# Kernel tuning notes

Measured on AMD Instinct MI355X. Metric: run time of the kernel, lower is better.

## Reference

```python
import jax, jax.numpy as jnp
import numpy as np

B, N, D, H, C, K = 4096, 64, 128, 256, 8, 3
L = N * D  # latent_dim = num_patches * d_model = 8192
UQ, LQ = 0.9, 0.1


def setup_inputs() -> dict:
    key = jax.random.key(0)
    ks = jax.random.split(key, 6)
    z = jax.random.normal(ks[0], (B, N, D), dtype=jnp.float32)
    q = jax.random.uniform(ks[1], (B,), dtype=jnp.float32)
    ch_ids = jax.random.randint(ks[2], (B,), 0, C, dtype=jnp.int32)
    # Xavier-style init for the 3 expert MLPs (Linear(L,H), Linear(H,L)) + heads Linear(L,1)
    s1 = float(np.sqrt(2.0 / (L + H)))
    s2 = float(np.sqrt(2.0 / (H + L)))
    sh = float(np.sqrt(2.0 / (L + 1)))
    W1 = jax.random.normal(ks[3], (K, L, H), dtype=jnp.float32) * s1
    W2 = jax.random.normal(ks[4], (K, H, L), dtype=jnp.float32) * s2
    Wh = jax.random.normal(ks[5], (K, L), dtype=jnp.float32) * sh
    return dict(z=z, q=q, ch_ids=ch_ids,
                W1=W1, b1=jnp.zeros((K, H), jnp.float32),
                W2=W2, b2=jnp.zeros((K, L), jnp.float32),
                Wh=Wh, bh=jnp.zeros((K,), jnp.float32))


def _channel_thresholds(q, ch_ids):
    """Per-channel sample-adjusted upper/lower quantiles, torch.quantile(..., interpolation='lower')."""
    def one(c):
        mask = ch_ids == c
        n = jnp.sum(mask).astype(jnp.float32)
        s = jnp.sort(jnp.where(mask, q, jnp.inf))  # channel values occupy first n slots
        au = jnp.ceil((n + 1.0) * UQ) / n
        pu = jnp.where(au > 1.0, UQ, au)
        al = jnp.floor((n + 1.0) * LQ) / n
        pl = jnp.where(al < 0.0, LQ, al)
        iu = jnp.floor(pu * (n - 1.0)).astype(jnp.int32)  # 'lower' interpolation index
        il = jnp.floor(pl * (n - 1.0)).astype(jnp.int32)
        return s[iu], s[il]
    return jax.vmap(one)(jnp.arange(C))  # (C,), (C,)


def reference(z, q, ch_ids, W1, b1, W2, b2, Wh, bh):
    uq_th, lq_th = _channel_thresholds(q, ch_ids)
    group = jnp.where(q <= lq_th[ch_ids], 2,
                      jnp.where(q >= uq_th[ch_ids], 0, 1)).astype(jnp.int32)  # (B,)
    zf = z.reshape(z.shape[0], -1)  # (B, L) -- Flatten(start_dim=-2)

    def expert(w1, c1, w2, c2, wh, ch):
        h = jax.nn.gelu(zf @ w1 + c1, approximate=False)   # (B, H)
        o = h @ w2 + c2                                     # (B, L)
        return o @ wh + ch                                  # (B,)

    logits_all = jax.vmap(expert)(W1, b1, W2, b2, Wh, bh)   # (K, B)
    logits = jnp.take_along_axis(logits_all, group[None, :], axis=0)[0]  # (B,)

    # per-channel softmax over logits (stable), matching torch.softmax on each channel's indices
    m = jax.ops.segment_max(logits, ch_ids, num_segments=C)
    e = jnp.exp(logits - m[ch_ids])
    ssum = jax.ops.segment_sum(e, ch_ids, num_segments=C)
    qwa_coeff = e / ssum[ch_ids]
    refined_probs = q * qwa_coeff
    return refined_probs
```

## Files before the change

### kernel.cpp

```cpp
#include <hip/hip_runtime.h>

typedef unsigned short u16;
typedef unsigned int u32;
typedef __attribute__((ext_vector_type(8))) short short8;
typedef __attribute__((ext_vector_type(4))) float f32x4;

#define NB 4096
#define LDIM 8192
#define HDIM 256
#define NEXP 3
#define NCH 8
#define KSPLIT 4
#define KSLICE (LDIM / KSPLIT)
#define BK 64
#define NT (KSLICE / BK)

__device__ inline u16 f2bf(float f) {
  u32 u = __float_as_uint(f);
  u += 0x7FFFu + ((u >> 16) & 1u);
  return (u16)(u >> 16);
}
__device__ inline u32 pack2(float x, float y) {
  return (u32)f2bf(x) | ((u32)f2bf(y) << 16);
}
__device__ inline void gll16(const void* g, void* l) {
  __builtin_amdgcn_global_load_lds((const __attribute__((address_space(1))) void*)g,
                                   (__attribute__((address_space(3))) void*)l, 16, 0, 0);
}

__global__ void thresh_kernel(const float* __restrict__ q, const int* __restrict__ ch,
                              float* __restrict__ uq_th, float* __restrict__ lq_th) {
  int c = blockIdx.x;
  int tid = threadIdx.x;
  __shared__ float vals[1536];
  __shared__ int oidx[1536];
  __shared__ int n_sh;
  if (tid == 0) n_sh = 0;
  __syncthreads();
  for (int i = tid; i < NB; i += 256) {
    if (ch[i] == c) {
      int p = atomicAdd(&n_sh, 1);
      if (p < 1536) { vals[p] = q[i]; oidx[p] = i; }
    }
  }
  __syncthreads();
  int n = n_sh < 1536 ? n_sh : 1536;
  float nf = (float)n_sh;
  float au = ceilf((nf + 1.0f) * 0.9f) / nf;
  float pu = (au > 1.0f) ? 0.9f : au;
  int iu = (int)floorf(pu * (nf - 1.0f));
  float al = floorf((nf + 1.0f) * 0.1f) / nf;
  float pl = (al < 0.0f) ? 0.1f : al;
  int il = (int)floorf(pl * (nf - 1.0f));
  for (int e = tid; e < n; e += 256) {
    float v = vals[e];
    int oi = oidx[e];
    int r = 0;
    for (int m = 0; m < n; ++m) {
      float vm = vals[m];
      if (vm < v || (vm == v && oidx[m] < oi)) r++;
    }
    if (r == iu) uq_th[c] = v;
    if (r == il) lq_th[c] = v;
  }
}

__global__ void group_kernel(const float* __restrict__ q, const int* __restrict__ ch,
                             const float* __restrict__ uq_th, const float* __restrict__ lq_th,
                             int* __restrict__ group, int* __restrict__ cnt, int* __restrict__ idxl) {
  int b = blockIdx.x * 256 + threadIdx.x;
  if (b >= NB) return;
  float qq = q[b];
  int c = ch[b];
  int g = (qq <= lq_th[c]) ? 2 : ((qq >= uq_th[c]) ? 0 : 1);
  group[b] = g;
  int pos = atomicAdd(&cnt[g], 1);
  idxl[g * NB + pos] = b;
}

__global__ void v_kernel(const float* __restrict__ W2, const float* __restrict__ Wh,
                         float* __restrict__ v) {
  int wv = blockIdx.x * 4 + (threadIdx.x >> 6);
  int lane = threadIdx.x & 63;
  int k = wv >> 8, h = wv & 255;
  const float4* w2 = (const float4*)(W2 + ((size_t)k * HDIM + h) * LDIM);
  const float4* wh = (const float4*)(Wh + (size_t)k * LDIM);
  float s = 0.f;
  for (int i = lane; i < LDIM / 4; i += 64) {
    float4 a = w2[i], b = wh[i];
    s += a.x * b.x + a.y * b.y + a.z * b.z + a.w * b.w;
  }
  for (int off = 32; off; off >>= 1) s += __shfl_down(s, off);
  if (lane == 0) v[k * HDIM + h] = s;
}

__global__ void cbias_kernel(const float* __restrict__ b2, const float* __restrict__ Wh,
                             const float* __restrict__ bh, float* __restrict__ cbias) {
  int k = threadIdx.x >> 6, lane = threadIdx.x & 63;
  float s = 0.f;
  for (int l = lane; l < LDIM; l += 64) s += b2[k * LDIM + l] * Wh[k * LDIM + l];
  for (int off = 32; off; off >>= 1) s += __shfl_down(s, off);
  if (lane == 0) cbias[k] = s + bh[k];
}

__global__ void transpose_kernel(const float* __restrict__ W1, u16* __restrict__ W1t) {
  __shared__ float tile[64][65];
  int k = blockIdx.z;
  int l0 = blockIdx.x * 64;
  int h0 = blockIdx.y * 64;
  int t = threadIdx.x;
  const float* src = W1 + (size_t)k * LDIM * HDIM + (size_t)l0 * HDIM + h0;
  u16* dst = W1t + (size_t)k * HDIM * LDIM + (size_t)h0 * LDIM + l0;
  int hr = t & 63, lr = t >> 6;
#pragma unroll
  for (int p = 0; p < 16; ++p) {
    int l = p * 4 + lr;
    tile[l][hr] = src[(size_t)l * HDIM + hr];
  }
  __syncthreads();
  int cw = t & 7, hw = t >> 3;
#pragma unroll
  for (int p = 0; p < 2; ++p) {
    int h = p * 32 + hw;
    short8 v8;
#pragma unroll
    for (int j = 0; j < 8; ++j) v8[j] = (short)f2bf(tile[cw * 8 + j][h]);
    *(short8*)&dst[(size_t)h * LDIM + cw * 8] = v8;
  }
}

__global__ void __launch_bounds__(256) gemm_kernel(
    const float* __restrict__ z, const u16* __restrict__ W1t,
    const int* __restrict__ idxl, const int* __restrict__ cnt,
    float* __restrict__ part) {
  int zid = blockIdx.z;
  int kexp = zid >> 2, s = zid & 3;
  int nk = cnt[kexp];
  int rowbase = blockIdx.x * 64;
  if (rowbase >= nk) return;
  int h0 = blockIdx.y * 64;
  int tid = threadIdx.x;
  int lane = tid & 63, wv = tid >> 6;

  __shared__ __align__(16) u16 As[2][4096];
  __shared__ __align__(16) u16 Bs[2][4096];
  __shared__ int sidx[64];

  const int* idxk = idxl + kexp * NB;
  if (tid < 64) {
    int p = rowbase + tid;
    sidx[tid] = idxk[p < nk ? p : nk - 1];
  }

  int r0 = tid >> 3, r1 = r0 + 32, kg = tid & 7;
  int p0 = rowbase + r0; if (p0 > nk - 1) p0 = nk - 1;
  int p1 = rowbase + r1; if (p1 > nk - 1) p1 = nk - 1;
  size_t kbase = (size_t)s * KSLICE;
  const float* zr0 = z + (size_t)idxk[p0] * LDIM + kbase + kg * 8;
  const float* zr1 = z + (size_t)idxk[p1] * LDIM + kbase + kg * 8;
  int swA0 = r0 * 64 + ((kg * 8) ^ ((r0 & 7) * 8));
  int swA1 = r1 * 64 + ((kg * 8) ^ ((r1 & 7) * 8));

  const u16* bsrc0 = W1t + ((size_t)kexp * HDIM + h0 + wv * 16 + (lane >> 3)) * LDIM +
                     kbase + (size_t)(((lane & 7) ^ (lane >> 3)) * 8);
  const u16* bsrc1 = bsrc0 + 8 * LDIM;

  int fr = lane & 15, kgl = (lane >> 4) * 8;
  int wr = (wv >> 1) * 32, wc = (wv & 1) * 32;
  int ra0 = wr + fr, ra1 = ra0 + 16, ca0 = wc + fr, ca1 = ca0 + 16;
  int xA0 = (ra0 & 7) * 8, xA1 = (ra1 & 7) * 8, xB0 = (ca0 & 7) * 8, xB1 = (ca1 & 7) * 8;

  f32x4 acc[2][2] = {};
  float4 a0, a1, a2, a3;

  {
    char* lb = (char*)&Bs[0][0] + wv * 2048;
    gll16(bsrc0, lb);
    gll16(bsrc1, lb + 1024);
    a0 = *(const float4*)(zr0);
    a1 = *(const float4*)(zr0 + 4);
    a2 = *(const float4*)(zr1);
    a3 = *(const float4*)(zr1 + 4);
    uint4 pa0, pa1;
    pa0.x = pack2(a0.x, a0.y); pa0.y = pack2(a0.z, a0.w);
    pa0.z = pack2(a1.x, a1.y); pa0.w = pack2(a1.z, a1.w);
    pa1.x = pack2(a2.x, a2.y); pa1.y = pack2(a2.z, a2.w);
    pa1.z = pack2(a3.x, a3.y); pa1.w = pack2(a3.z, a3.w);
    *(uint4*)&As[0][swA0] = pa0;
    *(uint4*)&As[0][swA1] = pa1;
  }
  __syncthreads();

  int cur = 0;
  for (int t = 0; t < NT; ++t) {
    int nxt = cur ^ 1;
    bool pre = (t + 1 < NT);
    if (pre) {
      int off = (t + 1) * BK;
      char* lb = (char*)&Bs[nxt][0] + wv * 2048;
      gll16(bsrc0 + off, lb);
      gll16(bsrc1 + off, lb + 1024);
      a0 = *(const float4*)(zr0 + off);
      a1 = *(const float4*)(zr0 + off + 4);
      a2 = *(const float4*)(zr1 + off);
      a3 = *(const float4*)(zr1 + off + 4);
    }
    const u16* Ac = &As[cur][0];
    const u16* Bc = &Bs[cur][0];
#pragma unroll
    for (int ks = 0; ks < 2; ++ks) {
      int kk = ks * 32 + kgl;
      short8 af0 = *(const short8*)&Ac[ra0 * 64 + (kk ^ xA0)];
      short8 af1 = *(const short8*)&Ac[ra1 * 64 + (kk ^ xA1)];
      short8 bf0 = *(const short8*)&Bc[ca0 * 64 + (kk ^ xB0)];
      short8 bf1 = *(const short8*)&Bc[ca1 * 64 + (kk ^ xB1)];
      acc[0][0] = __builtin_amdgcn_mfma_f32_16x16x32_bf16(af0, bf0, acc[0][0], 0, 0, 0);
      acc[0][1] = __builtin_amdgcn_mfma_f32_16x16x32_bf16(af0, bf1, acc[0][1], 0, 0, 0);
      acc[1][0] = __builtin_amdgcn_mfma_f32_16x16x32_bf16(af1, bf0, acc[1][0], 0, 0, 0);
      acc[1][1] = __builtin_amdgcn_mfma_f32_16x16x32_bf16(af1, bf1, acc[1][1], 0, 0, 0);
    }
    if (pre) {
      uint4 pa0, pa1;
      pa0.x = pack2(a0.x, a0.y); pa0.y = pack2(a0.z, a0.w);
      pa0.z = pack2(a1.x, a1.y); pa0.w = pack2(a1.z, a1.w);
      pa1.x = pack2(a2.x, a2.y); pa1.y = pack2(a2.z, a2.w);
      pa1.z = pack2(a3.x, a3.y); pa1.w = pack2(a3.z, a3.w);
      *(uint4*)&As[nxt][swA0] = pa0;
      *(uint4*)&As[nxt][swA1] = pa1;
    }
    __syncthreads();
    cur = nxt;
  }

  float* pdst = part + (size_t)s * NB * HDIM;
#pragma unroll
  for (int rb = 0; rb < 2; ++rb)
#pragma unroll
    for (int cb = 0; cb < 2; ++cb)
#pragma unroll
      for (int i = 0; i < 4; ++i) {
        int row = wr + rb * 16 + (lane >> 4) * 4 + i;
        int col = wc + cb * 16 + fr;
        if (rowbase + row < nk)
          pdst[(size_t)sidx[row] * HDIM + h0 + col] = acc[rb][cb][i];
      }
}

__global__ void ep_kernel(const float* __restrict__ part, const float* __restrict__ b1,
                          const float* __restrict__ v, const int* __restrict__ group,
                          float* __restrict__ logits) {
  int b = blockIdx.x;
  int t = threadIdx.x;
  int g = group[b];
  size_t o = (size_t)b * HDIM + t;
  const size_t SS = (size_t)NB * HDIM;
  float x = part[o] + part[o + SS] + part[o + 2 * SS] + part[o + 3 * SS] + b1[g * HDIM + t];
  float ge = 0.5f * x * (1.0f + erff(x * 0.70710678118654752f));
  float y = ge * v[g * HDIM + t];
#pragma unroll
  for (int off = 32; off; off >>= 1) y += __shfl_down(y, off);
  __shared__ float red[4];
  int lane = t & 63, wv = t >> 6;
  if (lane == 0) red[wv] = y;
  __syncthreads();
  if (t == 0) logits[b] = red[0] + red[1] + red[2] + red[3];
}

__global__ void softmax_kernel(const float* __restrict__ logits, const float* __restrict__ cbias,
                               const int* __restrict__ group, const float* __restrict__ q,
                               const int* __restrict__ ch, float* __restrict__ out) {
  int c = blockIdx.x;
  int tid = threadIdx.x;
  __shared__ float red[256];
  float m = -3.4e38f;
  for (int i = tid; i < NB; i += 256)
    if (ch[i] == c) {
      float x = logits[i] + cbias[group[i]];
      m = fmaxf(m, x);
    }
  red[tid] = m;
  __syncthreads();
  for (int s = 128; s > 0; s >>= 1) {
    if (tid < s) red[tid] = fmaxf(red[tid], red[tid + s]);
    __syncthreads();
  }
  m = red[0];
  __syncthreads();
  float sum = 0.f;
  for (int i = tid; i < NB; i += 256)
    if (ch[i] == c) sum += expf(logits[i] + cbias[group[i]] - m);
  red[tid] = sum;
  __syncthreads();
  for (int s = 128; s > 0; s >>= 1) {
    if (tid < s) red[tid] += red[tid + s];
    __syncthreads();
  }
  float S = red[0];
  for (int i = tid; i < NB; i += 256)
    if (ch[i] == c) out[i] = q[i] * expf(logits[i] + cbias[group[i]] - m) / S;
}

extern "C" void kernel_launch(void* const* d_in, const int* in_sizes, int n_in,
                              void* d_out, int out_size, void* d_ws, size_t ws_size,
                              hipStream_t stream) {
  const float* z  = (const float*)d_in[0];
  const float* q  = (const float*)d_in[1];
  const int*   ch = (const int*)d_in[2];
  const float* W1 = (const float*)d_in[3];
  const float* b1 = (const float*)d_in[4];
  const float* W2 = (const float*)d_in[5];
  const float* b2 = (const float*)d_in[6];
  const float* Wh = (const float*)d_in[7];
  const float* bh = (const float*)d_in[8];
  float* out = (float*)d_out;

  float* wsf    = (float*)d_ws;
  float* logits = wsf;
  int*   cnt    = (int*)(wsf + 4096);
  float* uq_th  = wsf + 4100;
  float* lq_th  = wsf + 4108;
  float* cbias  = wsf + 4116;
  float* v      = wsf + 4120;
  int*   group  = (int*)(wsf + 4888);
  int*   idxl   = (int*)(wsf + 8984);
  u16*   W1t    = (u16*)(wsf + 21272);
  float* part   = wsf + 3167000;

  hipMemsetAsync((char*)d_ws + 4096 * 4, 0, 16, stream);
  hipLaunchKernelGGL(thresh_kernel, dim3(NCH), dim3(256), 0, stream, q, ch, uq_th, lq_th);
  hipLaunchKernelGGL(group_kernel, dim3(16), dim3(256), 0, stream, q, ch, uq_th, lq_th, group, cnt, idxl);
  hipLaunchKernelGGL(v_kernel, dim3(192), dim3(256), 0, stream, W2, Wh, v);
  hipLaunchKernelGGL(cbias_kernel, dim3(1), dim3(192), 0, stream, b2, Wh, bh, cbias);
  hipLaunchKernelGGL(transpose_kernel, dim3(128, 4, 3), dim3(256), 0, stream, W1, W1t);
  hipLaunchKernelGGL(gemm_kernel, dim3(64, 4, NEXP * KSPLIT), dim3(256), 0, stream,
                     z, W1t, idxl, cnt, part);
  hipLaunchKernelGGL(ep_kernel, dim3(NB), dim3(256), 0, stream, part, b1, v, group, logits);
  hipLaunchKernelGGL(softmax_kernel, dim3(NCH), dim3(256), 0, stream, logits, cbias, group, q, ch, out);
}
```

Baseline: 542.2 us.

## Halve GEMM K-tile and raise split-K to eight slices when workspace allows

The gather-GEMM's K tile shrinks from 64 to 32, which halves LDS per block and gives each thread one A row chunk and one B load instead of two. A new swizzle matches the narrower tile. The split-K factor becomes a runtime value, eight when the workspace is large enough, to put more blocks in flight. The cost is more partial-sum traffic in the epilogue, which now loops over the slices, plus one sync per 32-wide step, so the fixed overhead per MFMA rises.

```diff
diff --git a/kernel.cpp b/kernel.cpp
--- a/kernel.cpp
+++ b/kernel.cpp
@@ -10,10 +10,7 @@
 #define HDIM 256
 #define NEXP 3
 #define NCH 8
-#define KSPLIT 4
-#define KSLICE (LDIM / KSPLIT)
-#define BK 64
-#define NT (KSLICE / BK)
+#define BK 32
 
 __device__ inline u16 f2bf(float f) {
   u32 u = __float_as_uint(f);
@@ -132,9 +129,9 @@
 __global__ void __launch_bounds__(256) gemm_kernel(
     const float* __restrict__ z, const u16* __restrict__ W1t,
     const int* __restrict__ idxl, const int* __restrict__ cnt,
-    float* __restrict__ part) {
+    float* __restrict__ part, int nsl, int nt) {
   int zid = blockIdx.z;
-  int kexp = zid >> 2, s = zid & 3;
+  int kexp = zid / nsl, s = zid - kexp * nsl;
   int nk = cnt[kexp];
   int rowbase = blockIdx.x * 64;
   if (rowbase >= nk) return;
@@ -142,8 +139,8 @@
   int tid = threadIdx.x;
   int lane = tid & 63, wv = tid >> 6;
 
-  __shared__ __align__(16) u16 As[2][4096];
-  __shared__ __align__(16) u16 Bs[2][4096];
+  __shared__ __align__(16) u16 As[2][2048];
+  __shared__ __align__(16) u16 Bs[2][2048];
   __shared__ int sidx[64];
 
   const int* idxk = idxl + kexp * NB;
@@ -152,81 +149,66 @@
     sidx[tid] = idxk[p < nk ? p : nk - 1];
   }
 
-  int r0 = tid >> 3, r1 = r0 + 32, kg = tid & 7;
-  int p0 = rowbase + r0; if (p0 > nk - 1) p0 = nk - 1;
-  int p1 = rowbase + r1; if (p1 > nk - 1) p1 = nk - 1;
-  size_t kbase = (size_t)s * KSLICE;
-  const float* zr0 = z + (size_t)idxk[p0] * LDIM + kbase + kg * 8;
-  const float* zr1 = z + (size_t)idxk[p1] * LDIM + kbase + kg * 8;
-  int swA0 = r0 * 64 + ((kg * 8) ^ ((r0 & 7) * 8));
-  int swA1 = r1 * 64 + ((kg * 8) ^ ((r1 & 7) * 8));
-
-  const u16* bsrc0 = W1t + ((size_t)kexp * HDIM + h0 + wv * 16 + (lane >> 3)) * LDIM +
-                     kbase + (size_t)(((lane & 7) ^ (lane >> 3)) * 8);
-  const u16* bsrc1 = bsrc0 + 8 * LDIM;
+  int row = tid >> 2, kg = tid & 3;
+  int p0 = rowbase + row; if (p0 > nk - 1) p0 = nk - 1;
+  int kslice = nt * BK;
+  size_t kbase = (size_t)s * kslice;
+  const float* zr = z + (size_t)idxk[p0] * LDIM + kbase + kg * 8;
+  int sch = kg ^ ((row >> 1) & 3);
+  int swA = row * BK + sch * 8;
+
+  const u16* bsrc = W1t + ((size_t)kexp * HDIM + h0 + row) * LDIM + kbase + sch * 8;
 
   int fr = lane & 15, kgl = (lane >> 4) * 8;
+  int kc = kgl >> 3;
   int wr = (wv >> 1) * 32, wc = (wv & 1) * 32;
   int ra0 = wr + fr, ra1 = ra0 + 16, ca0 = wc + fr, ca1 = ca0 + 16;
-  int xA0 = (ra0 & 7) * 8, xA1 = (ra1 & 7) * 8, xB0 = (ca0 & 7) * 8, xB1 = (ca1 & 7) * 8;
+  int oA0 = ra0 * BK + (kc ^ ((ra0 >> 1) & 3)) * 8;
+  int oA1 = ra1 * BK + (kc ^ ((ra1 >> 1) & 3)) * 8;
+  int oB0 = ca0 * BK + (kc ^ ((ca0 >> 1) & 3)) * 8;
+  int oB1 = ca1 * BK + (kc ^ ((ca1 >> 1) & 3)) * 8;
 
   f32x4 acc[2][2] = {};
-  float4 a0, a1, a2, a3;
-
+  float4 a0, a1;
+
+  gll16(bsrc, (char*)&Bs[0][0] + wv * 1024);
+  a0 = *(const float4*)(zr);
+  a1 = *(const float4*)(zr + 4);
   {
-    char* lb = (char*)&Bs[0][0] + wv * 2048;
-    gll16(bsrc0, lb);
-    gll16(bsrc1, lb + 1024);
-    a0 = *(const float4*)(zr0);
-    a1 = *(const float4*)(zr0 + 4);
-    a2 = *(const float4*)(zr1);
-    a3 = *(const float4*)(zr1 + 4);
-    uint4 pa0, pa1;
-    pa0.x = pack2(a0.x, a0.y); pa0.y = pack2(a0.z, a0.w);
-    pa0.z = pack2(a1.x, a1.y); pa0.w = pack2(a1.z, a1.w);
-    pa1.x = pack2(a2.x, a2.y); pa1.y = pack2(a2.z, a2.w);
-    pa1.z = pack2(a3.x, a3.y); pa1.w = pack2(a3.z, a3.w);
-    *(uint4*)&As[0][swA0] = pa0;
-    *(uint4*)&As[0][swA1] = pa1;
+    uint4 pa;
+    pa.x = pack2(a0.x, a0.y); pa.y = pack2(a0.z, a0.w);
+    pa.z = pack2(a1.x, a1.y); pa.w = pack2(a1.z, a1.w);
+    *(uint4*)&As[0][swA] = pa;
   }
   __syncthreads();
 
   int cur = 0;
-  for (int t = 0; t < NT; ++t) {
+  for (int t = 0; t < nt; ++t) {
     int nxt = cur ^ 1;
-    bool pre = (t + 1 < NT);
+    bool pre = (t + 1 < nt);
     if (pre) {
       int off = (t + 1) * BK;
-      char* lb = (char*)&Bs[nxt][0] + wv * 2048;
-      gll16(bsrc0 + off, lb);
-      gll16(bsrc1 + off, lb + 1024);
-      a0 = *(const float4*)(zr0 + off);
-      a1 = *(const float4*)(zr0 + off + 4);
-      a2 = *(const float4*)(zr1 + off);
-      a3 = *(const float4*)(zr1 + off + 4);
-    }
-    const u16* Ac = &As[cur][0];
-    const u16* Bc = &Bs[cur][0];
-#pragma unroll
-    for (int ks = 0; ks < 2; ++ks) {
-      int kk = ks * 32 + kgl;
-      short8 af0 = *(const short8*)&Ac[ra0 * 64 + (kk ^ xA0)];
-      short8 af1 = *(const short8*)&Ac[ra1 * 64 + (kk ^ xA1)];
-      short8 bf0 = *(const short8*)&Bc[ca0 * 64 + (kk ^ xB0)];
-      short8 bf1 = *(const short8*)&Bc[ca1 * 64 + (kk ^ xB1)];
+      gll16(bsrc + off, (char*)&Bs[nxt][0] + wv * 1024);
+      a0 = *(const float4*)(zr + off);
+      a1 = *(const float4*)(zr + off + 4);
+    }
+    {
+      const u16* Ac = &As[cur][0];
+      const u16* Bc = &Bs[cur][0];
+      short8 af0 = *(const short8*)&Ac[oA0];
+      short8 af1 = *(const short8*)&Ac[oA1];
+      short8 bf0 = *(const short8*)&Bc[oB0];
+      short8 bf1 = *(const short8*)&Bc[oB1];
       acc[0][0] = __builtin_amdgcn_mfma_f32_16x16x32_bf16(af0, bf0, acc[0][0], 0, 0, 0);
       acc[0][1] = __builtin_amdgcn_mfma_f32_16x16x32_bf16(af0, bf1, acc[0][1], 0, 0, 0);
       acc[1][0] = __builtin_amdgcn_mfma_f32_16x16x32_bf16(af1, bf0, acc[1][0], 0, 0, 0);
       acc[1][1] = __builtin_amdgcn_mfma_f32_16x16x32_bf16(af1, bf1, acc[1][1], 0, 0, 0);
     }
     if (pre) {
-      uint4 pa0, pa1;
-      pa0.x = pack2(a0.x, a0.y); pa0.y = pack2(a0.z, a0.w);
-      pa0.z = pack2(a1.x, a1.y); pa0.w = pack2(a1.z, a1.w);
-      pa1.x = pack2(a2.x, a2.y); pa1.y = pack2(a2.z, a2.w);
-      pa1.z = pack2(a3.x, a3.y); pa1.w = pack2(a3.z, a3.w);
-      *(uint4*)&As[nxt][swA0] = pa0;
-      *(uint4*)&As[nxt][swA1] = pa1;
+      uint4 pa;
+      pa.x = pack2(a0.x, a0.y); pa.y = pack2(a0.z, a0.w);
+      pa.z = pack2(a1.x, a1.y); pa.w = pack2(a1.z, a1.w);
+      *(uint4*)&As[nxt][swA] = pa;
     }
     __syncthreads();
     cur = nxt;
@@ -239,22 +221,23 @@
     for (int cb = 0; cb < 2; ++cb)
 #pragma unroll
       for (int i = 0; i < 4; ++i) {
-        int row = wr + rb * 16 + (lane >> 4) * 4 + i;
+        int r = wr + rb * 16 + (lane >> 4) * 4 + i;
         int col = wc + cb * 16 + fr;
-        if (rowbase + row < nk)
-          pdst[(size_t)sidx[row] * HDIM + h0 + col] = acc[rb][cb][i];
+        if (rowbase + r < nk)
+          pdst[(size_t)sidx[r] * HDIM + h0 + col] = acc[rb][cb][i];
       }
 }
 
 __global__ void ep_kernel(const float* __restrict__ part, const float* __restrict__ b1,
                           const float* __restrict__ v, const int* __restrict__ group,
-                          float* __restrict__ logits) {
+                          float* __restrict__ logits, int nsl) {
   int b = blockIdx.x;
   int t = threadIdx.x;
   int g = group[b];
   size_t o = (size_t)b * HDIM + t;
   const size_t SS = (size_t)NB * HDIM;
-  float x = part[o] + part[o + SS] + part[o + 2 * SS] + part[o + 3 * SS] + b1[g * HDIM + t];
+  float x = b1[g * HDIM + t];
+  for (int i = 0; i < nsl; ++i) x += part[o + i * SS];
   float ge = 0.5f * x * (1.0f + erff(x * 0.70710678118654752f));
   float y = ge * v[g * HDIM + t];
 #pragma unroll
@@ -326,14 +309,18 @@
   u16*   W1t    = (u16*)(wsf + 21272);
   float* part   = wsf + 3167000;
 
+  size_t need8 = (size_t)3167000 * 4 + (size_t)8 * NB * HDIM * 4;
+  int nsl = (ws_size >= need8) ? 8 : 4;
+  int nt = (LDIM / nsl) / BK;
+
   hipMemsetAsync((char*)d_ws + 4096 * 4, 0, 16, stream);
   hipLaunchKernelGGL(thresh_kernel, dim3(NCH), dim3(256), 0, stream, q, ch, uq_th, lq_th);
   hipLaunchKernelGGL(group_kernel, dim3(16), dim3(256), 0, stream, q, ch, uq_th, lq_th, group, cnt, idxl);
   hipLaunchKernelGGL(v_kernel, dim3(192), dim3(256), 0, stream, W2, Wh, v);
   hipLaunchKernelGGL(cbias_kernel, dim3(1), dim3(192), 0, stream, b2, Wh, bh, cbias);
   hipLaunchKernelGGL(transpose_kernel, dim3(128, 4, 3), dim3(256), 0, stream, W1, W1t);
-  hipLaunchKernelGGL(gemm_kernel, dim3(64, 4, NEXP * KSPLIT), dim3(256), 0, stream,
-                     z, W1t, idxl, cnt, part);
-  hipLaunchKernelGGL(ep_kernel, dim3(NB), dim3(256), 0, stream, part, b1, v, group, logits);
+  hipLaunchKernelGGL(gemm_kernel, dim3(64, 4, NEXP * nsl), dim3(256), 0, stream,
+                     z, W1t, idxl, cnt, part, nsl, nt);
+  hipLaunchKernelGGL(ep_kernel, dim3(NB), dim3(256), 0, stream, part, b1, v, group, logits, nsl);
   hipLaunchKernelGGL(softmax_kernel, dim3(NCH), dim3(256), 0, stream, logits, cbias, group, q, ch, out);
 }
```

After: 575.0 us. 6.0% more time.
